# Kernel optimization log

Measured on AMD Instinct MI355X. Metric: run time of the kernel, lower is better.

## Reference

```python
import jax, jax.numpy as jnp
import numpy as np

LORA_SCALING = 2.0


def setup_inputs() -> dict:
    key = jax.random.key(0)
    ks = jax.random.split(key, 12)
    B, S, H, F, E, R = 1, 2048, 2048, 8192, 8, 16
    s = 0.02  # small init so lora deltas stay numerically sane
    return {
        "hidden_states": jax.random.normal(ks[0], (B, S, H), jnp.float32),
        "gate_w": jax.random.normal(ks[1], (E, H), jnp.float32) * s,
        "Wg": jax.random.normal(ks[2], (F, H), jnp.float32) * s,
        "Wu": jax.random.normal(ks[3], (F, H), jnp.float32) * s,
        "Wd": jax.random.normal(ks[4], (H, F), jnp.float32) * s,
        "Ag": jax.random.normal(ks[5], (E, R, H), jnp.float32) * s,
        "Bg": jax.random.normal(ks[6], (E, F, R), jnp.float32) * s,
        "Au": jax.random.normal(ks[7], (E, R, H), jnp.float32) * s,
        "Bu": jax.random.normal(ks[8], (E, F, R), jnp.float32) * s,
        "Ad": jax.random.normal(ks[9], (E, R, F), jnp.float32) * s,
        "Bd": jax.random.normal(ks[10], (E, H, R), jnp.float32) * s,
        "top_k": 2,
    }


def reference(hidden_states, gate_w, Wg, Wu, Wd, Ag, Bg, Au, Bu, Ad, Bd, top_k):
    B, S, H = hidden_states.shape
    E = gate_w.shape[0]
    h = hidden_states.reshape(-1, H)  # [T, H]
    # router: softmax -> top-k -> renormalize
    logits = h @ gate_w.T                       # [T, E]
    rw = jax.nn.softmax(logits, axis=-1)
    rw_top, sel = jax.lax.top_k(rw, top_k)      # [T, K]
    rw_top = rw_top / jnp.sum(rw_top, axis=-1, keepdims=True)
    # per-token per-expert combine weight (0 if expert not selected)
    w_te = jnp.zeros((h.shape[0], E), h.dtype).at[
        jnp.arange(h.shape[0])[:, None], sel].add(rw_top)  # [T, E]
    # shared base projections computed once for all experts
    common_gate = h @ Wg.T   # [T, F]
    common_up = h @ Wu.T     # [T, F]
    out = jnp.zeros_like(h)
    for e in range(E):  # small fixed expert count; lora deltas are rank-16
        g = common_gate + LORA_SCALING * ((h @ Ag[e].T) @ Bg[e].T)
        u = common_up + LORA_SCALING * ((h @ Au[e].T) @ Bu[e].T)
        act = jax.nn.silu(g) * u                               # [T, F]
        d = act @ Wd.T + LORA_SCALING * ((act @ Ad[e].T) @ Bd[e].T)  # [T, H]
        out = out + w_te[:, e:e + 1] * d
    return out.reshape(B, S, H)
```

## Files before the change

kernel.cpp:

```cpp
#include <hip/hip_runtime.h>
#include <hip/hip_bf16.h>

typedef __attribute__((ext_vector_type(8))) short v8s;
typedef __attribute__((ext_vector_type(4))) float v4f;
typedef unsigned short u16;

static constexpr int TT = 2048;
static constexpr int HD = 2048;
static constexpr int FD = 8192;
static constexpr int NE = 8;
static constexpr int NR = 16;
static constexpr int NXE = 2*FD;
static constexpr int CU_OFF = FD;
static constexpr int KXD = FD + 512;

__device__ __forceinline__ u16 f2b(float f) {
  union { float f; unsigned u; } v; v.f = f;
  unsigned r = v.u + 0x7FFFu + ((v.u >> 16) & 1u);
  return (u16)(r >> 16);
}
__device__ __forceinline__ float b2f(u16 h) {
  union { unsigned u; float f; } v; v.u = ((unsigned)h) << 16;
  return v.f;
}
__device__ __forceinline__ v8s pack8(v4f a, v4f b) {
  v8s r;
  r[0]=(short)f2b(a.x); r[1]=(short)f2b(a.y); r[2]=(short)f2b(a.z); r[3]=(short)f2b(a.w);
  r[4]=(short)f2b(b.x); r[5]=(short)f2b(b.y); r[6]=(short)f2b(b.z); r[7]=(short)f2b(b.w);
  return r;
}
__device__ __forceinline__ void gload_lds16(const void* g, void* l) {
  __builtin_amdgcn_global_load_lds(
      (const __attribute__((address_space(1))) unsigned int*)g,
      (__attribute__((address_space(3))) unsigned int*)l, 16, 0, 0);
}
__device__ __forceinline__ void barrier_pin() {
  __builtin_amdgcn_s_barrier();
  __builtin_amdgcn_sched_barrier(0);
}
__device__ __forceinline__ void vm_wait4() { asm volatile("s_waitcnt vmcnt(4)" ::: "memory"); }
__device__ __forceinline__ void vm_wait0() { asm volatile("s_waitcnt vmcnt(0)" ::: "memory"); }

template<int Q>
__device__ __forceinline__ void mmq(v4f (&acc)[8][4], const v8s (&af)[2][2], const v8s (&bf)[4][2]) {
  __builtin_amdgcn_s_setprio(1);
  #pragma unroll
  for (int m2 = 0; m2 < 2; ++m2)
    #pragma unroll
    for (int nf = 0; nf < 4; ++nf) {
      acc[Q*2+m2][nf] = __builtin_amdgcn_mfma_f32_16x16x32_bf16(af[m2][0], bf[nf][0], acc[Q*2+m2][nf], 0, 0, 0);
      acc[Q*2+m2][nf] = __builtin_amdgcn_mfma_f32_16x16x32_bf16(af[m2][1], bf[nf][1], acc[Q*2+m2][nf], 0, 0, 0);
    }
  __builtin_amdgcn_s_setprio(0);
}

__global__ __launch_bounds__(256)
void cast_kernel(const float* __restrict__ src, u16* __restrict__ dst, long n) {
  long stride = (long)gridDim.x * 256 * 8;
  for (long i = ((long)blockIdx.x * 256 + threadIdx.x) * 8; i < n; i += stride) {
    v4f a = *(const v4f*)(src + i);
    v4f b = *(const v4f*)(src + i + 4);
    *(v8s*)(dst + i) = pack8(a, b);
  }
}

__global__ __launch_bounds__(256)
void cast_ld_kernel(const float* __restrict__ src, u16* __restrict__ dst,
                    int rows, int cols, int dld) {
  long total = (long)rows * (cols / 8);
  long stride = (long)gridDim.x * 256;
  for (long idx = (long)blockIdx.x * 256 + threadIdx.x; idx < total; idx += stride) {
    long r = idx / (cols / 8);
    int c8 = (int)(idx % (cols / 8)) * 8;
    v4f a = *(const v4f*)(src + r * cols + c8);
    v4f b = *(const v4f*)(src + r * cols + c8 + 4);
    *(v8s*)(dst + r * dld + c8) = pack8(a, b);
  }
}

__global__ __launch_bounds__(256)
void bdext_kernel(const float* __restrict__ Bd, u16* __restrict__ Wdx) {
  int idx = blockIdx.x * 256 + threadIdx.x;
  int hrow = idx >> 9, c = idx & 511;
  float v = 0.f;
  if (c < 128) {
    int e = c >> 4, r = c & 15;
    v = Bd[((size_t)e * HD + hrow) * 16 + r];
  }
  Wdx[(size_t)hrow * KXD + FD + c] = f2b(v);
}

__global__ __launch_bounds__(64)
void router_kernel(const float* __restrict__ h, const float* __restrict__ gw,
                   int* __restrict__ sel, int* __restrict__ count,
                   int* __restrict__ listTok, float* __restrict__ listW) {
  int t = blockIdx.x, lane = threadIdx.x;
  const float* hp = h + (size_t)t * HD;
  float acc[8] = {0,0,0,0,0,0,0,0};
  for (int i = lane; i < HD; i += 64) {
    float hv = hp[i];
    #pragma unroll
    for (int e = 0; e < 8; ++e) acc[e] += hv * gw[e*HD + i];
  }
  #pragma unroll
  for (int off = 32; off > 0; off >>= 1) {
    #pragma unroll
    for (int e = 0; e < 8; ++e) acc[e] += __shfl_xor(acc[e], off, 64);
  }
  if (lane == 0) {
    int e0 = -1, e1 = -1; float b0 = -1e30f, b1 = -1e30f;
    #pragma unroll
    for (int e = 0; e < 8; ++e) {
      float v = acc[e];
      if (v > b0) { b1 = b0; e1 = e0; b0 = v; e0 = e; }
      else if (v > b1) { b1 = v; e1 = e; }
    }
    float p1 = __expf(b1 - b0);
    float w0 = 1.f / (1.f + p1);
    float w1 = p1 * w0;
    sel[2*t] = e0; sel[2*t+1] = e1;
    int pos0 = atomicAdd(&count[e0], 1);
    listTok[e0*TT + pos0] = t;           listW[e0*TT + pos0] = w0;
    int pos1 = atomicAdd(&count[e1], 1);
    listTok[e1*TT + pos1] = t | (1<<20); listW[e1*TT + pos1] = w1;
  }
}

__global__ __launch_bounds__(256)
void gemm128a(const u16* __restrict__ A, const u16* __restrict__ B, float* __restrict__ Cout,
              int K, int ldc) {
  __shared__ u16 As[128*64];
  __shared__ u16 Bs[128*64];
  const int tid  = threadIdx.x;
  const int lane = tid & 63, wid = tid >> 6;
  const int gx = gridDim.x;
  const int lin = blockIdx.y * gx + blockIdx.x;
  const int chunk = (gx * gridDim.y) >> 3;
  const int wg = (lin & 7) * chunk + (lin >> 3);
  const int m0 = (wg % gx) * 128, n0 = (wg / gx) * 128;
  const int kc = K / gridDim.z;
  const int kbeg = blockIdx.z * kc;
  const int wr = wid >> 1, wc = wid & 1;
  const int lrow = lane >> 3, lcol = (lane & 7) * 8;
  v4f acc[4][4];
  #pragma unroll
  for (int mi = 0; mi < 4; ++mi)
    #pragma unroll
    for (int ni = 0; ni < 4; ++ni) acc[mi][ni] = (v4f){0.f,0.f,0.f,0.f};

  for (int k0 = kbeg; k0 < kbeg + kc; k0 += 64) {
    #pragma unroll
    for (int it = 0; it < 4; ++it) {
      int seg = wid*4 + it;
      int row = seg*8 + lrow;
      gload_lds16(A + (size_t)(m0+row)*K + k0 + lcol, As + seg*512);
      gload_lds16(B + (size_t)(n0+row)*K + k0 + lcol, Bs + seg*512);
    }
    __syncthreads();
    #pragma unroll
    for (int kk = 0; kk < 64; kk += 32) {
      v8s af[4], bfr[4];
      #pragma unroll
      for (int mi = 0; mi < 4; ++mi)
        af[mi] = *(const v8s*)(As + (wr*64 + mi*16 + (lane&15))*64 + kk + (lane>>4)*8);
      #pragma unroll
      for (int ni = 0; ni < 4; ++ni)
        bfr[ni] = *(const v8s*)(Bs + (wc*64 + ni*16 + (lane&15))*64 + kk + (lane>>4)*8);
      #pragma unroll
      for (int mi = 0; mi < 4; ++mi)
        #pragma unroll
        for (int ni = 0; ni < 4; ++ni)
          acc[mi][ni] = __builtin_amdgcn_mfma_f32_16x16x32_bf16(af[mi], bfr[ni], acc[mi][ni], 0, 0, 0);
    }
    __syncthreads();
  }

  #pragma unroll
  for (int mi = 0; mi < 4; ++mi)
    #pragma unroll
    for (int j = 0; j < 4; ++j) {
      int row = m0 + wr*64 + mi*16 + (lane>>4)*4 + j;
      size_t base = (size_t)row*ldc + n0 + wc*64 + (lane&15);
      #pragma unroll
      for (int ni = 0; ni < 4; ++ni)
        atomicAdd(&Cout[base + ni*16], acc[mi][ni][j]);
    }
}

template<int MODE>
__global__ __launch_bounds__(512, 2)
void gemm256(const u16* __restrict__ A, const u16* __restrict__ B, void* __restrict__ Cout,
             int ldk, int kchunk, int ldc) {
  __shared__ u16 lds[2][2][2][8192];
  const int tid = threadIdx.x, lane = tid & 63, wid = tid >> 6;
  const int gx = gridDim.x;
  const int nwg = gx * gridDim.y;
  const int lin = blockIdx.y * gx + blockIdx.x;
  const int chunk = nwg >> 3;
  const int wg = (lin & 7) * chunk + (lin >> 3);
  const int m0 = (wg % gx) * 256, n0 = (wg / gx) * 256;
  const long kbeg = (long)blockIdx.z * kchunk;
  const int NK = kchunk >> 6, NI = NK >> 1;
  const int wr = wid >> 2, wc = wid & 3;

  const int s_r = (wid << 4) + (lane >> 3);
  const int s_c = lane & 7;

  auto STAGE = [&](int slot, int ab, int half, const u16* M, int rc0, int kt) {
    const u16* g0 = M + (size_t)(rc0 + half*128 + s_r) * ldk + kbeg + kt*64 + ((s_c ^ (s_r & 7)) << 3);
    gload_lds16(g0, &lds[slot][ab][half][wid << 10]);
    const int r1 = s_r + 8;
    const u16* g1 = M + (size_t)(rc0 + half*128 + r1) * ldk + kbeg + kt*64 + ((s_c ^ (r1 & 7)) << 3);
    gload_lds16(g1, &lds[slot][ab][half][(wid << 10) + 512]);
  };
  auto LDA = [&](int slot, int mf, int c16b) -> v8s {
    int rr = (mf << 4) + (lane & 15);
    return *(const v8s*)&lds[slot][0][wr][rr*64 + (((c16b + (lane >> 4)) ^ (rr & 7)) << 3)];
  };
  auto LDB = [&](int slot, int nf, int c16b) -> v8s {
    int row = (wc << 6) + (nf << 4) + (lane & 15);
    int rr = row & 127;
    return *(const v8s*)&lds[slot][1][row >> 7][rr*64 + (((c16b + (lane >> 4)) ^ (rr & 7)) << 3)];
  };

  v4f acc[8][4];
  #pragma unroll
  for (int mf = 0; mf < 8; ++mf)
    #pragma unroll
    for (int nf = 0; nf < 4; ++nf) acc[mf][nf] = (v4f){0.f,0.f,0.f,0.f};

  STAGE(0,1,0,B,n0,0); STAGE(0,1,1,B,n0,0);
  STAGE(0,0,0,A,m0,0); STAGE(0,0,1,A,m0,0);
  STAGE(1,1,0,B,n0,1); STAGE(1,1,1,B,n0,1);
  vm_wait4();
  barrier_pin();

  for (int i = 0; i < NI; ++i) {
    const int kt0 = 2*i, kt1 = kt0 + 1;
    const int kt2c = (kt0 + 2 < NK) ? kt0 + 2 : kt0;
    const bool s45 = (kt0 + 2 < NK), s67 = (kt1 + 2 < NK);
    v8s bf[4][2], af[2][2];
    #pragma unroll
    for (int nf = 0; nf < 4; ++nf) { bf[nf][0] = LDB(0,nf,0); bf[nf][1] = LDB(0,nf,4); }
    af[0][0]=LDA(0,0,0); af[0][1]=LDA(0,0,4); af[1][0]=LDA(0,1,0); af[1][1]=LDA(0,1,4);
    STAGE(1,0,0,A,m0,kt1);
    barrier_pin(); mmq<0>(acc,af,bf); barrier_pin();
    af[0][0]=LDA(0,2,0); af[0][1]=LDA(0,2,4); af[1][0]=LDA(0,3,0); af[1][1]=LDA(0,3,4);
    STAGE(1,0,1,A,m0,kt1);
    barrier_pin(); mmq<1>(acc,af,bf); barrier_pin();
    af[0][0]=LDA(0,4,0); af[0][1]=LDA(0,4,4); af[1][0]=LDA(0,5,0); af[1][1]=LDA(0,5,4);
    STAGE(0,1,0,B,n0,kt2c);
    barrier_pin(); mmq<2>(acc,af,bf); barrier_pin();
    af[0][0]=LDA(0,6,0); af[0][1]=LDA(0,6,4); af[1][0]=LDA(0,7,0); af[1][1]=LDA(0,7,4);
    STAGE(0,1,1,B,n0,kt2c);
    vm_wait4();
    barrier_pin(); mmq<3>(acc,af,bf); barrier_pin();
    #pragma unroll
    for (int nf = 0; nf < 4; ++nf) { bf[nf][0] = LDB(1,nf,0); bf[nf][1] = LDB(1,nf,4); }
    af[0][0]=LDA(1,0,0); af[0][1]=LDA(1,0,4); af[1][0]=LDA(1,1,0); af[1][1]=LDA(1,1,4);
    if (s45) STAGE(0,0,0,A,m0,kt0+2);
    barrier_pin(); mmq<0>(acc,af,bf); barrier_pin();
    af[0][0]=LDA(1,2,0); af[0][1]=LDA(1,2,4); af[1][0]=LDA(1,3,0); af[1][1]=LDA(1,3,4);
    if (s45) STAGE(0,0,1,A,m0,kt0+2);
    barrier_pin(); mmq<1>(acc,af,bf); barrier_pin();
    af[0][0]=LDA(1,4,0); af[0][1]=LDA(1,4,4); af[1][0]=LDA(1,5,0); af[1][1]=LDA(1,5,4);
    if (s67) STAGE(1,1,0,B,n0,kt1+2);
    barrier_pin(); mmq<2>(acc,af,bf); barrier_pin();
    af[0][0]=LDA(1,6,0); af[0][1]=LDA(1,6,4); af[1][0]=LDA(1,7,0); af[1][1]=LDA(1,7,4);
    if (s67) STAGE(1,1,1,B,n0,kt1+2);
    vm_wait4();
    barrier_pin(); mmq<3>(acc,af,bf); barrier_pin();
  }
  vm_wait0();

  if (MODE == 0) {
    u16* C = (u16*)Cout;
    #pragma unroll
    for (int mf = 0; mf < 8; ++mf)
      #pragma unroll
      for (int j = 0; j < 4; ++j) {
        int row = m0 + wr*128 + mf*16 + (lane>>4)*4 + j;
        size_t base = (size_t)row*ldc + n0 + wc*64 + (lane&15);
        #pragma unroll
        for (int nf = 0; nf < 4; ++nf)
          C[base + nf*16] = f2b(acc[mf][nf][j]);
      }
  } else {
    float* C = (float*)Cout;
    #pragma unroll
    for (int mf = 0; mf < 8; ++mf)
      #pragma unroll
      for (int j = 0; j < 4; ++j) {
        int row = m0 + wr*128 + mf*16 + (lane>>4)*4 + j;
        size_t base = (size_t)row*ldc + n0 + wc*64 + (lane&15);
        #pragma unroll
        for (int nf = 0; nf < 4; ++nf)
          atomicAdd(&C[base + nf*16], acc[mf][nf][j]);
      }
  }
}

static constexpr int HA_LD = 40;
static constexpr int BG_LD = 40;
static constexpr int AW_LD = 72;
static constexpr int CT_LD = 72;

__global__ __launch_bounds__(256)
void expert_kernel(const u16* __restrict__ CGU,
                   const float* __restrict__ hAx,
                   const float* __restrict__ Bg, const float* __restrict__ Bu,
                   const float* __restrict__ Ad,
                   const int* __restrict__ count, const int* __restrict__ listTok,
                   const float* __restrict__ listW,
                   u16* __restrict__ actw0, u16* __restrict__ actw1,
                   float* __restrict__ cC) {
  const int e = blockIdx.y, g = blockIdx.x, fb = blockIdx.z;
  const int n = count[e];
  if (g*16 >= n) return;
  const int tid = threadIdx.x, lane = tid & 63, w = tid >> 6;
  __shared__ u16 hAg[16*HA_LD], hAu[16*HA_LD];
  __shared__ u16 BS[4][64*BG_LD];
  __shared__ u16 AWs[4][16*AW_LD];
  __shared__ u16 cgT[4][16*CT_LD], cuT[4][16*CT_LD];
  __shared__ int sTok[16], sSlot[16];
  __shared__ float sW[16];
  __shared__ float dAred[4][256];

  if (tid < 16) {
    int idx = g*16 + tid;
    if (idx < n) {
      int ent = listTok[e*TT + idx];
      sTok[tid] = ent & 0xFFFF; sSlot[tid] = (ent >> 20) & 1; sW[tid] = listW[e*TT + idx];
    } else { sTok[tid] = TT; sSlot[tid] = 0; sW[tid] = 0.f; }
  }
  __syncthreads();
  if (tid < 128) {
    int tensor = tid >> 6;
    int sub = tid & 63;
    int row = sub >> 2, c8 = (sub & 3) * 8;
    int trd = min(sTok[row], TT - 1);
    u16 vals[8];
    if (c8 < 16) {
      const float* src = hAx + (size_t)trd*256 + tensor*128 + e*NR + c8;
      v4f a = *(const v4f*)src, b = *(const v4f*)(src + 4);
      v8s p = pack8(a, b);
      #pragma unroll
      for (int q = 0; q < 8; ++q) vals[q] = (u16)p[q];
    } else {
      #pragma unroll
      for (int q = 0; q < 8; ++q) vals[q] = 0;
    }
    u16* dst = (tensor ? hAu : hAg) + row*HA_LD + c8;
    #pragma unroll
    for (int q = 0; q < 8; ++q) dst[q] = vals[q];
  }
  __syncthreads();

  int tR[4], slR[4]; float wR[4];
  #pragma unroll
  for (int j = 0; j < 4; ++j) {
    int r = (lane>>4)*4 + j;
    tR[j] = sTok[r]; slR[j] = sSlot[r]; wR[j] = sW[r];
  }
  v8s afg = *(const v8s*)(hAg + (lane&15)*HA_LD + (lane>>4)*8);
  v8s afu = *(const v8s*)(hAu + (lane&15)*HA_LD + (lane>>4)*8);
  v4f accDA = (v4f){0.f,0.f,0.f,0.f};
  u16* bsw = BS[w]; u16* aww = AWs[w]; u16* cgw = cgT[w]; u16* cuw = cuT[w];

  {
    v8s z = {0,0,0,0,0,0,0,0};
    *(v8s*)(bsw + lane*BG_LD + 16) = z; *(v8s*)(bsw + lane*BG_LD + 24) = z;
  }

  const int ch_end = fb*32 + 32;
  for (int ch = fb*32 + w; ch < ch_end; ch += 4) {
    int f0 = ch * 64;
    {
      int srow = lane >> 3, c8 = (lane & 7) * 8;
      #pragma unroll
      for (int rr = 0; rr < 2; ++rr) {
        int row = srow + rr*8;
        size_t trd = (size_t)min(sTok[row], TT - 1);
        *(v8s*)(cgw + row*CT_LD + c8) = *(const v8s*)(CGU + trd*NXE + f0 + c8);
        *(v8s*)(cuw + row*CT_LD + c8) = *(const v8s*)(CGU + trd*NXE + CU_OFF + f0 + c8);
      }
    }
    v4f dg[4], du[4];
    {
      const float* gp = Bg + ((size_t)e*FD + f0 + lane)*16;
      v4f q0 = *(const v4f*)gp, q1 = *(const v4f*)(gp+4), q2 = *(const v4f*)(gp+8), q3 = *(const v4f*)(gp+12);
      *(v8s*)(bsw + lane*BG_LD)     = pack8(q0, q1);
      *(v8s*)(bsw + lane*BG_LD + 8) = pack8(q2, q3);
      #pragma unroll
      for (int nf = 0; nf < 4; ++nf) {
        v8s bgf = *(const v8s*)(bsw + (nf*16 + (lane&15))*BG_LD + (lane>>4)*8);
        dg[nf] = __builtin_amdgcn_mfma_f32_16x16x32_bf16(afg, bgf, (v4f){0.f,0.f,0.f,0.f}, 0, 0, 0);
      }
    }
    {
      const float* up = Bu + ((size_t)e*FD + f0 + lane)*16;
      v4f r0 = *(const v4f*)up, r1 = *(const v4f*)(up+4), r2 = *(const v4f*)(up+8), r3 = *(const v4f*)(up+12);
      *(v8s*)(bsw + lane*BG_LD)     = pack8(r0, r1);
      *(v8s*)(bsw + lane*BG_LD + 8) = pack8(r2, r3);
      #pragma unroll
      for (int nf = 0; nf < 4; ++nf) {
        v8s buf = *(const v8s*)(bsw + (nf*16 + (lane&15))*BG_LD + (lane>>4)*8);
        du[nf] = __builtin_amdgcn_mfma_f32_16x16x32_bf16(afu, buf, (v4f){0.f,0.f,0.f,0.f}, 0, 0, 0);
      }
    }
    #pragma unroll
    for (int nf = 0; nf < 4; ++nf) {
      #pragma unroll
      for (int j = 0; j < 4; ++j) {
        int rj = (lane>>4)*4 + j;
        int fi = nf*16 + (lane&15);
        float cgv = b2f(cgw[rj*CT_LD + fi]);
        float cuv = b2f(cuw[rj*CT_LD + fi]);
        float gv = cgv + 2.f * dg[nf][j];
        float uv = cuv + 2.f * du[nf][j];
        float a  = gv / (1.f + __expf(-gv)) * uv;
        u16 ab = f2b(wR[j] * a);
        (slR[j] ? actw1 : actw0)[(size_t)tR[j]*FD + f0 + fi] = ab;
        aww[rj*AW_LD + fi] = ab;
      }
    }
    #pragma unroll
    for (int ks = 0; ks < 2; ++ks) {
      v8s aA = *(const v8s*)(aww + (lane&15)*AW_LD + ks*32 + (lane>>4)*8);
      const float* ap = Ad + ((size_t)e*16 + (lane&15))*FD + f0 + ks*32 + (lane>>4)*8;
      v4f q0 = *(const v4f*)ap, q1 = *(const v4f*)(ap+4);
      v8s bA = pack8(q0, q1);
      accDA = __builtin_amdgcn_mfma_f32_16x16x32_bf16(aA, bA, accDA, 0, 0, 0);
    }
  }
  #pragma unroll
  for (int j = 0; j < 4; ++j)
    dAred[w][((lane>>4)*4 + j)*16 + (lane&15)] = accDA[j];
  __syncthreads();
  {
    int row = tid >> 4, col = tid & 15;
    float s2 = dAred[0][row*16+col] + dAred[1][row*16+col] + dAred[2][row*16+col] + dAred[3][row*16+col];
    atomicAdd(&cC[((size_t)sTok[row]*2 + sSlot[row])*16 + col], 2.f * s2);
  }
}

__global__ __launch_bounds__(256)
void combine2_kernel(const u16* __restrict__ a0, const u16* __restrict__ a1,
                     const float* __restrict__ cC, const int* __restrict__ sel,
                     u16* __restrict__ abx) {
  int t = blockIdx.x, tid = threadIdx.x;
  const u16* p0 = a0 + (size_t)t * FD;
  const u16* p1 = a1 + (size_t)t * FD;
  u16* po = abx + (size_t)t * KXD;
  for (int i = tid * 8; i < FD; i += 256 * 8) {
    v8s x = *(const v8s*)(p0 + i);
    v8s y = *(const v8s*)(p1 + i);
    v8s o;
    #pragma unroll
    for (int j = 0; j < 8; ++j) o[j] = (short)f2b(b2f((u16)x[j]) + b2f((u16)y[j]));
    *(v8s*)(po + i) = o;
  }
  for (int c = tid; c < 512; c += 256) {
    float v = 0.f;
    if (c < 128) {
      int e_i = c >> 4, r = c & 15;
      if (sel[2*t]     == e_i) v += cC[((size_t)t*2 + 0)*16 + r];
      if (sel[2*t + 1] == e_i) v += cC[((size_t)t*2 + 1)*16 + r];
    }
    po[FD + c] = f2b(v);
  }
}

extern "C" void kernel_launch(void* const* d_in, const int* in_sizes, int n_in,
                              void* d_out, int out_size, void* d_ws, size_t ws_size,
                              hipStream_t stream) {
  (void)in_sizes; (void)n_in; (void)out_size; (void)ws_size;
  const float* h  = (const float*)d_in[0];
  const float* gw = (const float*)d_in[1];
  const float* Wg = (const float*)d_in[2];
  const float* Wu = (const float*)d_in[3];
  const float* Wd = (const float*)d_in[4];
  const float* Ag = (const float*)d_in[5];
  const float* Bg = (const float*)d_in[6];
  const float* Au = (const float*)d_in[7];
  const float* Bu = (const float*)d_in[8];
  const float* Ad = (const float*)d_in[9];
  const float* Bd = (const float*)d_in[10];

  char* ws = (char*)d_ws;
  size_t off = 0;
  auto alloc = [&](size_t bytes) { size_t c = off; off += (bytes + 255) & ~(size_t)255; return c; };
  u16*  hb     = (u16*)(ws + alloc((size_t)TT*HD*2));
  u16*  Bgux   = (u16*)(ws + alloc((size_t)(TT+1)*FD*2*2));
  u16*  Agu    = (u16*)(ws + alloc((size_t)256*HD*2));
  u16*  Wdx    = (u16*)(ws + alloc((size_t)HD*KXD*2));
  u16*  CGU    = (u16*)(ws + alloc((size_t)TT*NXE*2));
  float* hAx   = (float*)(ws + alloc((size_t)TT*256*4));
  float* cC    = (float*)(ws + alloc((size_t)(TT+1)*2*16*4));
  int*  sel    = (int*)(ws + alloc((size_t)TT*2*4));
  int*  count  = (int*)(ws + alloc(256));
  int*  listTok= (int*)(ws + alloc((size_t)NE*TT*4));
  float* listW = (float*)(ws + alloc((size_t)NE*TT*4));
  u16*  actw0  = Bgux;
  u16*  actw1  = Bgux + (size_t)(TT+1)*FD;
  u16*  abx    = CGU;

  hipMemsetAsync(count, 0, NE*sizeof(int), stream);
  hipMemsetAsync(cC, 0, (size_t)(TT+1)*2*16*4, stream);
  hipMemsetAsync(hAx, 0, (size_t)TT*256*4, stream);
  hipMemsetAsync(d_out, 0, (size_t)TT*HD*4, stream);

  cast_kernel<<<2048, 256, 0, stream>>>(h,  hb,  (long)TT*HD);
  cast_kernel<<<4096, 256, 0, stream>>>(Wg, Bgux, (long)FD*HD);
  cast_kernel<<<4096, 256, 0, stream>>>(Wu, Bgux + (size_t)FD*HD, (long)FD*HD);
  cast_kernel<<<128,  256, 0, stream>>>(Ag, Agu, (long)NE*NR*HD);
  cast_kernel<<<128,  256, 0, stream>>>(Au, Agu + (size_t)128*HD, (long)NE*NR*HD);
  cast_ld_kernel<<<4096, 256, 0, stream>>>(Wd, Wdx, HD, FD, KXD);
  bdext_kernel<<<4096, 256, 0, stream>>>(Bd, Wdx);

  router_kernel<<<TT, 64, 0, stream>>>(h, gw, sel, count, listTok, listW);

  gemm128a<<<dim3(16, 2, 8), 256, 0, stream>>>(hb, Agu, hAx, HD, 256);

  gemm256<0><<<dim3(8, 64, 1), 512, 0, stream>>>(hb, Bgux, CGU, HD, HD, NXE);

  expert_kernel<<<dim3(128, NE, 4), 256, 0, stream>>>(CGU, hAx, Bg, Bu, Ad, count, listTok, listW,
                                                      actw0, actw1, cC);

  combine2_kernel<<<TT, 256, 0, stream>>>(actw0, actw1, cC, sel, abx);

  gemm256<2><<<dim3(8, 8, 4), 512, 0, stream>>>(abx, Wdx, d_out, KXD, KXD/4, HD);
}
```

Measured before the change: 516.8 us.

## Fuse all weight casts and zero-fills into one prep kernel; pre-cast LoRA B/A to bf16

Merges the separate cast, strided-cast, Bd-extension kernels and two memsets into a single large prep kernel, with block ranges assigned to each sub-task. Bg, Bu and Ad are also pre-cast to bf16 so the expert kernel loads MFMA fragments straight from global memory. This removes the LDS staging buffer and the per-chunk fp32→bf16 packing there. The intent is fewer launches and less per-block conversion work, at the cost of extra workspace and a few more global loads of bf16 LoRA weights.

```diff
diff --git a/kernel.cpp b/kernel.cpp
--- a/kernel.cpp
+++ b/kernel.cpp
@@ -54,40 +54,70 @@
   __builtin_amdgcn_s_setprio(0);
 }
 
+static constexpr int PREP_BLOCKS = 31232;
 __global__ __launch_bounds__(256)
-void cast_kernel(const float* __restrict__ src, u16* __restrict__ dst, long n) {
-  long stride = (long)gridDim.x * 256 * 8;
-  for (long i = ((long)blockIdx.x * 256 + threadIdx.x) * 8; i < n; i += stride) {
-    v4f a = *(const v4f*)(src + i);
-    v4f b = *(const v4f*)(src + i + 4);
-    *(v8s*)(dst + i) = pack8(a, b);
-  }
-}
-
-__global__ __launch_bounds__(256)
-void cast_ld_kernel(const float* __restrict__ src, u16* __restrict__ dst,
-                    int rows, int cols, int dld) {
-  long total = (long)rows * (cols / 8);
-  long stride = (long)gridDim.x * 256;
-  for (long idx = (long)blockIdx.x * 256 + threadIdx.x; idx < total; idx += stride) {
-    long r = idx / (cols / 8);
-    int c8 = (int)(idx % (cols / 8)) * 8;
-    v4f a = *(const v4f*)(src + r * cols + c8);
-    v4f b = *(const v4f*)(src + r * cols + c8 + 4);
-    *(v8s*)(dst + r * dld + c8) = pack8(a, b);
-  }
-}
-
-__global__ __launch_bounds__(256)
-void bdext_kernel(const float* __restrict__ Bd, u16* __restrict__ Wdx) {
-  int idx = blockIdx.x * 256 + threadIdx.x;
-  int hrow = idx >> 9, c = idx & 511;
-  float v = 0.f;
-  if (c < 128) {
-    int e = c >> 4, r = c & 15;
-    v = Bd[((size_t)e * HD + hrow) * 16 + r];
-  }
-  Wdx[(size_t)hrow * KXD + FD + c] = f2b(v);
+void prep_kernel(const float* __restrict__ h, const float* __restrict__ Wg,
+                 const float* __restrict__ Wu, const float* __restrict__ Wd,
+                 const float* __restrict__ Ag, const float* __restrict__ Au,
+                 const float* __restrict__ Bg, const float* __restrict__ Bu,
+                 const float* __restrict__ Ad, const float* __restrict__ Bd,
+                 u16* __restrict__ hb, u16* __restrict__ Bgux, u16* __restrict__ Agu,
+                 u16* __restrict__ Wdx, u16* __restrict__ Bgb, u16* __restrict__ Bub,
+                 u16* __restrict__ Adb, float* __restrict__ outz, float* __restrict__ hAx) {
+  const int b = blockIdx.x, tid = threadIdx.x;
+  if (b < 2048) {
+    long i = ((long)b*256 + tid)*8;
+    *(v8s*)(hb+i) = pack8(*(const v4f*)(h+i), *(const v4f*)(h+i+4));
+  } else if (b < 10240) {
+    long i = ((long)(b-2048)*256 + tid)*8;
+    *(v8s*)(Bgux+i) = pack8(*(const v4f*)(Wg+i), *(const v4f*)(Wg+i+4));
+  } else if (b < 18432) {
+    long i = ((long)(b-10240)*256 + tid)*8;
+    *(v8s*)(Bgux+(size_t)FD*HD+i) = pack8(*(const v4f*)(Wu+i), *(const v4f*)(Wu+i+4));
+  } else if (b < 26624) {
+    long idx = (long)(b-18432)*256 + tid;
+    long r = idx >> 10;
+    int c8 = (int)(idx & 1023) * 8;
+    const float* s = Wd + r*FD + c8;
+    *(v8s*)(Wdx + r*KXD + c8) = pack8(*(const v4f*)s, *(const v4f*)(s+4));
+  } else if (b < 26752) {
+    long i = ((long)(b-26624)*256 + tid)*8;
+    *(v8s*)(Agu+i) = pack8(*(const v4f*)(Ag+i), *(const v4f*)(Ag+i+4));
+  } else if (b < 26880) {
+    long i = ((long)(b-26752)*256 + tid)*8;
+    *(v8s*)(Agu+(size_t)128*HD+i) = pack8(*(const v4f*)(Au+i), *(const v4f*)(Au+i+4));
+  } else if (b < 27392) {
+    long i = ((long)(b-26880)*256 + tid)*8;
+    *(v8s*)(Bgb+i) = pack8(*(const v4f*)(Bg+i), *(const v4f*)(Bg+i+4));
+  } else if (b < 27904) {
+    long i = ((long)(b-27392)*256 + tid)*8;
+    *(v8s*)(Bub+i) = pack8(*(const v4f*)(Bu+i), *(const v4f*)(Bu+i+4));
+  } else if (b < 28416) {
+    long i = ((long)(b-27904)*256 + tid)*8;
+    *(v8s*)(Adb+i) = pack8(*(const v4f*)(Ad+i), *(const v4f*)(Ad+i+4));
+  } else if (b < 28928) {
+    long idx = (long)(b-28416)*256 + tid;
+    int hrow = (int)(idx >> 6);
+    int c8 = (int)(idx & 63) * 8;
+    v8s o;
+    if (c8 < 128) {
+      int e = c8 >> 4, r0 = c8 & 15;
+      const float* s = Bd + ((size_t)e*HD + hrow)*16 + r0;
+      o = pack8(*(const v4f*)s, *(const v4f*)(s+4));
+    } else {
+      #pragma unroll
+      for (int q = 0; q < 8; ++q) o[q] = 0;
+    }
+    *(v8s*)(Wdx + (size_t)hrow*KXD + FD + c8) = o;
+  } else if (b < 30976) {
+    long i = ((long)(b-28928)*256 + tid)*8;
+    v4f z = {0.f,0.f,0.f,0.f};
+    *(v4f*)(outz+i) = z; *(v4f*)(outz+i+4) = z;
+  } else {
+    long i = ((long)(b-30976)*256 + tid)*8;
+    v4f z = {0.f,0.f,0.f,0.f};
+    *(v4f*)(hAx+i) = z; *(v4f*)(hAx+i+4) = z;
+  }
 }
 
 __global__ __launch_bounds__(64)
@@ -301,15 +331,14 @@
 }
 
 static constexpr int HA_LD = 40;
-static constexpr int BG_LD = 40;
 static constexpr int AW_LD = 72;
 static constexpr int CT_LD = 72;
 
 __global__ __launch_bounds__(256)
 void expert_kernel(const u16* __restrict__ CGU,
                    const float* __restrict__ hAx,
-                   const float* __restrict__ Bg, const float* __restrict__ Bu,
-                   const float* __restrict__ Ad,
+                   const u16* __restrict__ Bgb, const u16* __restrict__ Bub,
+                   const u16* __restrict__ Adb,
                    const int* __restrict__ count, const int* __restrict__ listTok,
                    const float* __restrict__ listW,
                    u16* __restrict__ actw0, u16* __restrict__ actw1,
@@ -319,7 +348,6 @@
   if (g*16 >= n) return;
   const int tid = threadIdx.x, lane = tid & 63, w = tid >> 6;
   __shared__ u16 hAg[16*HA_LD], hAu[16*HA_LD];
-  __shared__ u16 BS[4][64*BG_LD];
   __shared__ u16 AWs[4][16*AW_LD];
   __shared__ u16 cgT[4][16*CT_LD], cuT[4][16*CT_LD];
   __shared__ int sTok[16], sSlot[16];
@@ -362,15 +390,15 @@
     int r = (lane>>4)*4 + j;
     tR[j] = sTok[r]; slR[j] = sSlot[r]; wR[j] = sW[r];
   }
-  v8s afg = *(const v8s*)(hAg + (lane&15)*HA_LD + (lane>>4)*8);
-  v8s afu = *(const v8s*)(hAu + (lane&15)*HA_LD + (lane>>4)*8);
+  const int khalf = lane >> 4;
+  v8s afg = *(const v8s*)(hAg + (lane&15)*HA_LD + khalf*8);
+  v8s afu = *(const v8s*)(hAu + (lane&15)*HA_LD + khalf*8);
   v4f accDA = (v4f){0.f,0.f,0.f,0.f};
-  u16* bsw = BS[w]; u16* aww = AWs[w]; u16* cgw = cgT[w]; u16* cuw = cuT[w];
-
-  {
-    v8s z = {0,0,0,0,0,0,0,0};
-    *(v8s*)(bsw + lane*BG_LD + 16) = z; *(v8s*)(bsw + lane*BG_LD + 24) = z;
-  }
+  u16* aww = AWs[w]; u16* cgw = cgT[w]; u16* cuw = cuT[w];
+  const v8s zero8 = {0,0,0,0,0,0,0,0};
+  const u16* BgE = Bgb + (size_t)e*FD*16;
+  const u16* BuE = Bub + (size_t)e*FD*16;
+  const u16* AdE = Adb + (size_t)e*16*FD;
 
   const int ch_end = fb*32 + 32;
   for (int ch = fb*32 + w; ch < ch_end; ch += 4) {
@@ -386,27 +414,13 @@
       }
     }
     v4f dg[4], du[4];
-    {
-      const float* gp = Bg + ((size_t)e*FD + f0 + lane)*16;
-      v4f q0 = *(const v4f*)gp, q1 = *(const v4f*)(gp+4), q2 = *(const v4f*)(gp+8), q3 = *(const v4f*)(gp+12);
-      *(v8s*)(bsw + lane*BG_LD)     = pack8(q0, q1);
-      *(v8s*)(bsw + lane*BG_LD + 8) = pack8(q2, q3);
-      #pragma unroll
-      for (int nf = 0; nf < 4; ++nf) {
-        v8s bgf = *(const v8s*)(bsw + (nf*16 + (lane&15))*BG_LD + (lane>>4)*8);
-        dg[nf] = __builtin_amdgcn_mfma_f32_16x16x32_bf16(afg, bgf, (v4f){0.f,0.f,0.f,0.f}, 0, 0, 0);
-      }
-    }
-    {
-      const float* up = Bu + ((size_t)e*FD + f0 + lane)*16;
-      v4f r0 = *(const v4f*)up, r1 = *(const v4f*)(up+4), r2 = *(const v4f*)(up+8), r3 = *(const v4f*)(up+12);
-      *(v8s*)(bsw + lane*BG_LD)     = pack8(r0, r1);
-      *(v8s*)(bsw + lane*BG_LD + 8) = pack8(r2, r3);
-      #pragma unroll
-      for (int nf = 0; nf < 4; ++nf) {
-        v8s buf = *(const v8s*)(bsw + (nf*16 + (lane&15))*BG_LD + (lane>>4)*8);
-        du[nf] = __builtin_amdgcn_mfma_f32_16x16x32_bf16(afu, buf, (v4f){0.f,0.f,0.f,0.f}, 0, 0, 0);
-      }
+    #pragma unroll
+    for (int nf = 0; nf < 4; ++nf) {
+      int f = f0 + nf*16 + (lane & 15);
+      v8s bgf = (khalf < 2) ? *(const v8s*)(BgE + (size_t)f*16 + khalf*8) : zero8;
+      dg[nf] = __builtin_amdgcn_mfma_f32_16x16x32_bf16(afg, bgf, (v4f){0.f,0.f,0.f,0.f}, 0, 0, 0);
+      v8s buf = (khalf < 2) ? *(const v8s*)(BuE + (size_t)f*16 + khalf*8) : zero8;
+      du[nf] = __builtin_amdgcn_mfma_f32_16x16x32_bf16(afu, buf, (v4f){0.f,0.f,0.f,0.f}, 0, 0, 0);
     }
     #pragma unroll
     for (int nf = 0; nf < 4; ++nf) {
@@ -426,10 +440,8 @@
     }
     #pragma unroll
     for (int ks = 0; ks < 2; ++ks) {
-      v8s aA = *(const v8s*)(aww + (lane&15)*AW_LD + ks*32 + (lane>>4)*8);
-      const float* ap = Ad + ((size_t)e*16 + (lane&15))*FD + f0 + ks*32 + (lane>>4)*8;
-      v4f q0 = *(const v4f*)ap, q1 = *(const v4f*)(ap+4);
-      v8s bA = pack8(q0, q1);
+      v8s aA = *(const v8s*)(aww + (lane&15)*AW_LD + ks*32 + khalf*8);
+      v8s bA = *(const v8s*)(AdE + (size_t)(lane&15)*FD + f0 + ks*32 + khalf*8);
       accDA = __builtin_amdgcn_mfma_f32_16x16x32_bf16(aA, bA, accDA, 0, 0, 0);
     }
   }
@@ -495,6 +507,9 @@
   u16*  Agu    = (u16*)(ws + alloc((size_t)256*HD*2));
   u16*  Wdx    = (u16*)(ws + alloc((size_t)HD*KXD*2));
   u16*  CGU    = (u16*)(ws + alloc((size_t)TT*NXE*2));
+  u16*  Bgb    = (u16*)(ws + alloc((size_t)NE*FD*16*2));
+  u16*  Bub    = (u16*)(ws + alloc((size_t)NE*FD*16*2));
+  u16*  Adb    = (u16*)(ws + alloc((size_t)NE*16*FD*2));
   float* hAx   = (float*)(ws + alloc((size_t)TT*256*4));
   float* cC    = (float*)(ws + alloc((size_t)(TT+1)*2*16*4));
   int*  sel    = (int*)(ws + alloc((size_t)TT*2*4));
@@ -507,16 +522,10 @@
 
   hipMemsetAsync(count, 0, NE*sizeof(int), stream);
   hipMemsetAsync(cC, 0, (size_t)(TT+1)*2*16*4, stream);
-  hipMemsetAsync(hAx, 0, (size_t)TT*256*4, stream);
-  hipMemsetAsync(d_out, 0, (size_t)TT*HD*4, stream);
-
-  cast_kernel<<<2048, 256, 0, stream>>>(h,  hb,  (long)TT*HD);
-  cast_kernel<<<4096, 256, 0, stream>>>(Wg, Bgux, (long)FD*HD);
-  cast_kernel<<<4096, 256, 0, stream>>>(Wu, Bgux + (size_t)FD*HD, (long)FD*HD);
-  cast_kernel<<<128,  256, 0, stream>>>(Ag, Agu, (long)NE*NR*HD);
-  cast_kernel<<<128,  256, 0, stream>>>(Au, Agu + (size_t)128*HD, (long)NE*NR*HD);
-  cast_ld_kernel<<<4096, 256, 0, stream>>>(Wd, Wdx, HD, FD, KXD);
-  bdext_kernel<<<4096, 256, 0, stream>>>(Bd, Wdx);
+
+  prep_kernel<<<PREP_BLOCKS, 256, 0, stream>>>(h, Wg, Wu, Wd, Ag, Au, Bg, Bu, Ad, Bd,
+                                               hb, Bgux, Agu, Wdx, Bgb, Bub, Adb,
+                                               (float*)d_out, hAx);
 
   router_kernel<<<TT, 64, 0, stream>>>(h, gw, sel, count, listTok, listW);
 
@@ -524,7 +533,7 @@
 
   gemm256<0><<<dim3(8, 64, 1), 512, 0, stream>>>(hb, Bgux, CGU, HD, HD, NXE);
 
-  expert_kernel<<<dim3(128, NE, 4), 256, 0, stream>>>(CGU, hAx, Bg, Bu, Ad, count, listTok, listW,
+  expert_kernel<<<dim3(128, NE, 4), 256, 0, stream>>>(CGU, hAx, Bgb, Bub, Adb, count, listTok, listW,
                                                       actw0, actw1, cC);
 
   combine2_kernel<<<TT, 256, 0, stream>>>(actw0, actw1, cC, sel, abx);
```

After: 508.4 us. Within noise of the previous version (-1.6%).
